# Performance work log

Hardware: AMD Instinct MI355X
Metric: run time of the kernel (lower is better)

## Reference

```python
import jax, jax.numpy as jnp
import numpy as np

NUM_CLASSES = 81
THRESHOLD = 0.5
NEGPOS_RATIO = 3
VARIANCE = (0.1, 0.2)
B, P, O = 32, 24564, 50


def point_form(pr):
    # center-form (cx,cy,w,h) -> corner-form (x1,y1,x2,y2)
    return jnp.concatenate([pr[:, :2] - pr[:, 2:] / 2, pr[:, :2] + pr[:, 2:] / 2], axis=1)


def jaccard(a, b):
    # a: [O,4] corner-form truths, b: [P,4] corner-form priors -> [O,P]
    lt = jnp.maximum(a[:, None, :2], b[None, :, :2])
    rb = jnp.minimum(a[:, None, 2:], b[None, :, 2:])
    wh = jnp.clip(rb - lt, 0.0)
    inter = wh[..., 0] * wh[..., 1]
    area_a = ((a[:, 2] - a[:, 0]) * (a[:, 3] - a[:, 1]))[:, None]
    area_b = ((b[:, 2] - b[:, 0]) * (b[:, 3] - b[:, 1]))[None, :]
    return inter / (area_a + area_b - inter)


def encode(matched, priors_cf):
    # matched: [P,4] corner-form gt; priors_cf: [P,4] center-form
    g_cxcy = ((matched[:, :2] + matched[:, 2:]) / 2 - priors_cf[:, :2]) / (VARIANCE[0] * priors_cf[:, 2:])
    g_wh = jnp.log((matched[:, 2:] - matched[:, :2]) / priors_cf[:, 2:]) / VARIANCE[1]
    return jnp.concatenate([g_cxcy, g_wh], axis=1)


def match_one(truths, labels, priors_cf, priors_pf):
    ov = jaccard(truths, priors_pf)                       # [O,P]
    best_prior_idx = jnp.argmax(ov, axis=1)               # [O] best prior per truth
    best_truth_overlap = jnp.max(ov, axis=0)              # [P]
    best_truth_idx = jnp.argmax(ov, axis=0)               # [P]
    # ensure every gt matches its best prior
    best_truth_overlap = best_truth_overlap.at[best_prior_idx].set(2.0)
    best_truth_idx = best_truth_idx.at[best_prior_idx].set(jnp.arange(truths.shape[0]))
    matches = truths[best_truth_idx]                      # [P,4]
    conf = labels[best_truth_idx] + 1                     # background = 0
    conf = jnp.where(best_truth_overlap < THRESHOLD, 0, conf)
    loc = encode(matches, priors_cf)
    return loc, conf


def setup_inputs() -> dict:
    key = jax.random.key(0)
    k1, k2, k3, k4, k5, k6, k7 = jax.random.split(key, 7)
    loc_data = jax.random.normal(k1, (B, P, 4), jnp.float32)
    conf_data = jax.random.normal(k2, (B, P, NUM_CLASSES), jnp.float32)
    cxcy = jax.random.uniform(k3, (P, 2), minval=0.05, maxval=0.95)
    wh = jax.random.uniform(k4, (P, 2), minval=0.05, maxval=0.5)
    priors = jnp.concatenate([cxcy, wh], axis=1).astype(jnp.float32)
    gc = jax.random.uniform(k5, (B, O, 2), minval=0.1, maxval=0.9)
    gwh = jax.random.uniform(k6, (B, O, 2), minval=0.05, maxval=0.4)
    boxes = jnp.clip(jnp.concatenate([gc - gwh / 2, gc + gwh / 2], axis=-1), 0.0, 1.0)
    labels = jax.random.randint(k7, (B, O), 0, NUM_CLASSES - 1).astype(jnp.float32)
    targets = jnp.concatenate([boxes, labels[..., None]], axis=-1).astype(jnp.float32)
    return {"loc_data": loc_data, "conf_data": conf_data, "priors": priors, "targets": targets}


def reference(loc_data, conf_data, priors, targets):
    truths = targets[..., :4]                              # [B,O,4]
    labels = targets[..., 4].astype(jnp.int32)             # [B,O]
    priors_pf = point_form(priors)
    loc_t, conf_t = jax.vmap(match_one, in_axes=(0, 0, None, None))(truths, labels, priors, priors_pf)
    pos = conf_t > 0                                       # [B,P]

    # localization smooth-L1 over positives (sum reduction)
    diff = loc_data - loc_t
    sl1 = jnp.where(jnp.abs(diff) < 1.0, 0.5 * diff * diff, jnp.abs(diff) - 0.5)
    loss_l = jnp.sum(sl1 * pos[..., None].astype(sl1.dtype))

    # per-anchor CE loss for hard negative mining
    lse = jax.nn.logsumexp(conf_data, axis=-1)             # [B,P]
    gathered = jnp.take_along_axis(conf_data, conf_t[..., None], axis=-1)[..., 0]
    loss_c_all = lse - gathered                            # [B,P]
    loss_c_mine = jnp.where(pos, 0.0, loss_c_all)
    loss_idx = jnp.argsort(-loss_c_mine, axis=1)
    idx_rank = jnp.argsort(loss_idx, axis=1)
    num_pos = jnp.sum(pos.astype(jnp.int32), axis=1, keepdims=True)  # [B,1]
    num_neg = jnp.minimum(NEGPOS_RATIO * num_pos, P - 1)
    neg = idx_rank < num_neg                               # [B,P]

    sel = jnp.logical_or(pos, neg)
    loss_c = jnp.sum(jnp.where(sel, loss_c_all, 0.0))

    N = jnp.sum(num_pos).astype(loss_l.dtype)
    return loss_l / N, loss_c / N
```

## Files before the change

### kernel.cpp

```cpp
#include <hip/hip_runtime.h>

#define NB 32
#define NP 24564
#define NO 50
#define NC 81
#define THR 0.5f
#define KA_CHUNK 1024
#define NCH 24

__device__ __forceinline__ float rl_f(float v, int j) {
  return __uint_as_float((unsigned)__builtin_amdgcn_readlane((int)__float_as_uint(v), j));
}
__device__ __forceinline__ float bp_f(float v, int j4) {
  return __uint_as_float((unsigned)__builtin_amdgcn_ds_bpermute(j4, (int)__float_as_uint(v)));
}


__global__ __launch_bounds__(256) void kA(
    const float* __restrict__ priors, const float* __restrict__ targets,
    unsigned long long* __restrict__ bpc,
    double* __restrict__ acc, int* __restrict__ num_pos,
    float* __restrict__ accLb, float* __restrict__ accCb,
    int* __restrict__ done) {
  __shared__ float4 s_pf[KA_CHUNK];
  __shared__ float s_t[NO * 5];
  __shared__ unsigned long long s_bp[256];
  const int b = blockIdx.y;
  const int tid = threadIdx.x;
  const int base = blockIdx.x * KA_CHUNK;

  if (blockIdx.x == 0 && b == 0) {
    if (tid < 4) acc[tid] = 0.0;
    else if (tid >= 32 && tid < 64) num_pos[tid - 32] = 0;
    else if (tid >= 64 && tid < 96) accLb[tid - 64] = 0.0f;
    else if (tid >= 96 && tid < 128) accCb[tid - 96] = 0.0f;
    else if (tid == 128) *done = 0;
  }

  for (int i = tid; i < NO * 5; i += 256) s_t[i] = targets[b * NO * 5 + i];

  #pragma unroll
  for (int k = 0; k < KA_CHUNK / 256; ++k) {
    const int p = base + k * 256 + tid;
    float4 pf;
    if (p < NP) {
      const float4 pr = ((const float4*)priors)[p];
      pf = make_float4(pr.x - pr.z * 0.5f, pr.y - pr.w * 0.5f,
                       pr.x + pr.z * 0.5f, pr.y + pr.w * 0.5f);
    } else {
      pf = make_float4(3.0f, 3.0f, 3.0f, 3.0f);
    }
    s_pf[k * 256 + tid] = pf;
  }
  __syncthreads();

  const int wv = tid >> 6;
  const int lane = tid & 63;
  unsigned long long best = 0ull;
  if (lane < NO) {
    const float tx1 = s_t[lane * 5 + 0], ty1 = s_t[lane * 5 + 1];
    const float tx2 = s_t[lane * 5 + 2], ty2 = s_t[lane * 5 + 3];
    const float area_a = (tx2 - tx1) * (ty2 - ty1);
    const int i0 = wv * 256;
    #pragma unroll 8
    for (int i = 0; i < 256; ++i) {
      const float4 q = s_pf[i0 + i];
      const float wx = fmaxf(fminf(q.z, tx2) - fmaxf(q.x, tx1), 0.0f);
      const float wy = fmaxf(fminf(q.w, ty2) - fmaxf(q.y, ty1), 0.0f);
      const float inter = wx * wy;
      const float ab = (q.z - q.x) * (q.w - q.y);
      const float iou = __fdividef(inter, area_a + ab - inter);
      const unsigned p = (unsigned)(base + i0 + i);
      const unsigned long long pk =
          (((unsigned long long)__float_as_uint(iou)) << 32) |
          (unsigned long long)(0xFFFFFFFFu - p);
      if (pk > best) best = pk;
    }
  }
  s_bp[tid] = best;
  __syncthreads();
  if (tid < NO) {
    unsigned long long m = s_bp[tid];
    unsigned long long v = s_bp[64 + tid];  if (v > m) m = v;
    v = s_bp[128 + tid];                    if (v > m) m = v;
    v = s_bp[192 + tid];                    if (v > m) m = v;
    bpc[(size_t)(b * NO + tid) * NCH + blockIdx.x] = m;
  }
}

__global__ __launch_bounds__(256) void kMS(
    const float* __restrict__ loc, const float* __restrict__ conf,
    const float* __restrict__ priors, const float* __restrict__ targets,
    const unsigned long long* __restrict__ bpc,
    float* __restrict__ mine, int* __restrict__ num_pos,
    float* __restrict__ accLb, float* __restrict__ accCb) {
  __shared__ float s_s[256];
  __shared__ int s_tpb[NO];
  __shared__ float sLw[4], sCw[4];
  __shared__ int sNw[4];
  const int tid = threadIdx.x;
  const int lane = tid & 63;
  const int b = blockIdx.y;
  const int rowbase = blockIdx.x * 256 + (tid & 192);
  const int p = rowbase + lane;
  const bool valid = (p < NP);
  const int pc = valid ? p : NP - 1;
  const size_t grow = (size_t)b * NP + pc;
  const float* tb = targets + (size_t)b * (NO * 5);

  if (tid < NO) {
    const unsigned long long* sl = bpc + (size_t)(b * NO + tid) * NCH;
    unsigned long long m = 0ull;
    #pragma unroll
    for (int c = 0; c < NCH; ++c) {
      const unsigned long long v = sl[c];
      if (v > m) m = v;
    }
    s_tpb[tid] = (int)(0xFFFFFFFFu - (unsigned)(m & 0xFFFFFFFFull));
  }

  float ttx1 = 3.f, tty1 = 3.f, ttx2 = 3.f, tty2 = 3.f, tar = 0.f, tlab = 0.f;
  if (lane < NO) {
    ttx1 = tb[lane * 5 + 0]; tty1 = tb[lane * 5 + 1];
    ttx2 = tb[lane * 5 + 2]; tty2 = tb[lane * 5 + 3];
    tlab = tb[lane * 5 + 4];
    tar = (ttx2 - ttx1) * (tty2 - tty1);
  }
  const float4 pr = ((const float4*)priors)[pc];
  const float4 ldv = ((const float4*)loc)[grow];
  const float px1 = pr.x - pr.z * 0.5f, py1 = pr.y - pr.w * 0.5f;
  const float px2 = pr.x + pr.z * 0.5f, py2 = pr.y + pr.w * 0.5f;
  const float areab = (px2 - px1) * (py2 - py1);
  __syncthreads();
  const int tpb = (lane < NO) ? s_tpb[lane] : -1;

  const int l16 = lane & 15;
  const int g4 = (lane >> 4) & 3;
  const int c0 = (4 - g4) & 3;
  const int tc = (l16 < c0) ? l16 : (c0 + 64 + (l16 - c0));
  const float* cb = conf + (size_t)b * NP * NC;

  float4 v4[8];
  float vta[8], v80[8];

  #define KMS_ROWP(ph) (cb + (size_t)((rowbase + (ph) * 4 + g4) < NP \
      ? (rowbase + (ph) * 4 + g4) : (NP - 1)) * NC)
  #define KMS_ISSUE(ph) { const float* rp_ = KMS_ROWP(ph);            \
      v4[(ph) & 7] = *(const float4*)(rp_ + c0 + 4 * l16);            \
      vta[(ph) & 7] = rp_[tc]; v80[(ph) & 7] = rp_[80]; }

  KMS_ISSUE(0) KMS_ISSUE(1) KMS_ISSUE(2)
  KMS_ISSUE(3) KMS_ISSUE(4) KMS_ISSUE(5)
  __builtin_amdgcn_sched_barrier(0);

  float bv = -1.0f;
  int bj = 0;
  #pragma unroll 2
  for (int j = 0; j < NO; ++j) {
    const float x1 = rl_f(ttx1, j), y1 = rl_f(tty1, j);
    const float x2 = rl_f(ttx2, j), y2 = rl_f(tty2, j);
    const float aa = rl_f(tar, j);
    const float wx = fmaxf(fminf(x2, px2) - fmaxf(x1, px1), 0.0f);
    const float wy = fmaxf(fminf(y2, py2) - fmaxf(y1, py1), 0.0f);
    const float inter = wx * wy;
    const float iou = __fdividef(inter, aa + areab - inter);
    if (iou > bv) { bv = iou; bj = j; }
  }

  int ovj = -1;
  unsigned long long M = __ballot((lane < NO) && ((unsigned)(tpb - rowbase) < 64u));
  while (M) {
    const int l = __ffsll((long long)M) - 1;
    M &= M - 1;
    const int r = __builtin_amdgcn_readlane(tpb, l) - rowbase;
    if (lane == r) ovj = l;
  }
  const int jm = (ovj >= 0) ? ovj : bj;
  const bool pos = valid && ((ovj >= 0) || (bv >= THR));
  const int j4 = jm << 2;
  const float lab = bp_f(tlab, j4);
  const float mx1 = bp_f(ttx1, j4), my1 = bp_f(tty1, j4);
  const float mx2 = bp_f(ttx2, j4), my2 = bp_f(tty2, j4);
  const int conft = pos ? ((int)lab + 1) : 0;

  float sl1 = 0.0f;
  if (pos) {
    const float gcx = __fdividef((mx1 + mx2) * 0.5f - pr.x, 0.1f * pr.z);
    const float gcy = __fdividef((my1 + my2) * 0.5f - pr.y, 0.1f * pr.w);
    const float gw = __logf(__fdividef(mx2 - mx1, pr.z)) * 5.0f;
    const float gh = __logf(__fdividef(my2 - my1, pr.w)) * 5.0f;
    const float d0 = ldv.x - gcx, d1 = ldv.y - gcy;
    const float d2 = ldv.z - gw, d3 = ldv.w - gh;
    #pragma unroll
    for (int q = 0; q < 4; ++q) {
      const float d = (q == 0) ? d0 : (q == 1) ? d1 : (q == 2) ? d2 : d3;
      const float a = fabsf(d);
      sl1 += (a < 1.0f) ? 0.5f * d * d : a - 0.5f;
    }
  }

  #pragma unroll
  for (int ph = 0; ph < 16; ++ph) {
    if (ph + 6 < 16) KMS_ISSUE(ph + 6)
    const float4 v = v4[ph & 7];
    float s = __expf(v.x) + __expf(v.y) + __expf(v.z) + __expf(v.w);
    s += __expf(vta[ph & 7]);
    const float e80 = __expf(v80[ph & 7]);
    s += (l16 == 0) ? e80 : 0.0f;
    s += __shfl_xor(s, 1, 64);
    s += __shfl_xor(s, 2, 64);
    s += __shfl_xor(s, 4, 64);
    s += __shfl_xor(s, 8, 64);
    if (l16 == 0) s_s[(tid & 192) + ph * 4 + g4] = s;
  }
  const float myS = s_s[tid];

  const float gval = conf[grow * NC + conft];
  const float lca = __logf(myS) - gval;

  float sumL = 0.0f, sumC = 0.0f;
  int cnt = 0;
  if (valid) {
    mine[grow] = pos ? 0.0f : fmaxf(lca, 0.0f);
    if (pos) { cnt = 1; sumC = lca; sumL = sl1; }
  }

  #pragma unroll
  for (int m = 1; m <= 32; m <<= 1) {
    sumL += __shfl_xor(sumL, m, 64);
    sumC += __shfl_xor(sumC, m, 64);
    cnt  += __shfl_xor(cnt, m, 64);
  }
  const int w = tid >> 6;
  if (lane == 0) { sLw[w] = sumL; sCw[w] = sumC; sNw[w] = cnt; }
  __syncthreads();
  if (tid == 0) {
    const float L = sLw[0] + sLw[1] + sLw[2] + sLw[3];
    const float C = sCw[0] + sCw[1] + sCw[2] + sCw[3];
    const int n = sNw[0] + sNw[1] + sNw[2] + sNw[3];
    if (L != 0.0f) atomicAdd(&accLb[b], L);
    if (C != 0.0f) atomicAdd(&accCb[b], C);
    if (n) atomicAdd(&num_pos[b], n);
  }
}

__global__ __launch_bounds__(512) void kD(
    const float* __restrict__ mine, const int* __restrict__ num_pos,
    double* __restrict__ acc, int* __restrict__ done,
    const float* __restrict__ accLb, const float* __restrict__ accCb,
    float* __restrict__ out) {
  const int b = blockIdx.x;
  const int tid = threadIdx.x;
  const uint4* vb4 = (const uint4*)(mine + (size_t)b * NP);

  unsigned vals[48];
  #pragma unroll
  for (int k = 0; k < 12; ++k) {
    const int i = tid + k * 512;
    uint4 q = make_uint4(0u, 0u, 0u, 0u);
    if (i < NP / 4) q = vb4[i];
    vals[4 * k + 0] = q.x; vals[4 * k + 1] = q.y;
    vals[4 * k + 2] = q.z; vals[4 * k + 3] = q.w;
  }

  const int K = min(3 * num_pos[b], NP - 1);

  __shared__ int s_w[2][8];
  unsigned prefix = 0u;
  int remaining = K;

  for (int bit = 30; bit >= 0; --bit) {
    const unsigned want = (prefix >> bit) | 1u;
    int cnt = 0;
    #pragma unroll
    for (int k = 0; k < 48; ++k) cnt += ((vals[k] >> bit) == want) ? 1 : 0;
    #pragma unroll
    for (int m = 32; m >= 1; m >>= 1) cnt += __shfl_xor(cnt, m, 64);
    const int buf = bit & 1;
    if ((tid & 63) == 0) s_w[buf][tid >> 6] = cnt;
    __syncthreads();
    int total = 0;
    #pragma unroll
    for (int w = 0; w < 8; ++w) total += s_w[buf][w];
    if (total >= remaining) prefix |= (1u << bit);
    else remaining -= total;
  }

  if (K > 0) {
    const float t = __uint_as_float(prefix);
    double sg = 0.0;
    int cg = 0;
    #pragma unroll
    for (int k = 0; k < 48; ++k) {
      const float f = __uint_as_float(vals[k]);
      if (f > t) { sg += (double)f; cg++; }
    }
    #pragma unroll
    for (int m = 32; m >= 1; m >>= 1) {
      sg += __shfl_xor(sg, m, 64);
      cg += __shfl_xor(cg, m, 64);
    }
    __shared__ double s_sd[8];
    __shared__ int s_sc[8];
    const int wid = tid >> 6;
    if ((tid & 63) == 0) { s_sd[wid] = sg; s_sc[wid] = cg; }
    __syncthreads();
    if (tid == 0) {
      double S = 0.0;
      int C = 0;
      for (int w = 0; w < 8; ++w) { S += s_sd[w]; C += s_sc[w]; }
      S += (double)(K - C) * (double)t;
      atomicAdd(&acc[2], S);
    }
  }

  __shared__ int s_last;
  __syncthreads();
  if (tid == 0) {
    __threadfence();
    s_last = (atomicAdd(done, 1) == NB - 1) ? 1 : 0;
  }
  __syncthreads();
  if (s_last && tid < 64) {
    int n = 0;
    float L = 0.0f, C = 0.0f;
    if (tid < NB) { n = num_pos[tid]; L = accLb[tid]; C = accCb[tid]; }
    #pragma unroll
    for (int m = 32; m >= 1; m >>= 1) {
      n += __shfl_xor(n, m, 64);
      L += __shfl_xor(L, m, 64);
      C += __shfl_xor(C, m, 64);
    }
    if (tid == 0) {
      const double S = atomicAdd(&acc[2], 0.0);
      const double Nf = (double)n;
      out[0] = (float)((double)L / Nf);
      out[1] = (float)(((double)C + S) / Nf);
    }
  }
}

extern "C" void kernel_launch(void* const* d_in, const int* in_sizes, int n_in,
                              void* d_out, int out_size, void* d_ws, size_t ws_size,
                              hipStream_t stream) {
  const float* loc     = (const float*)d_in[0];
  const float* conf    = (const float*)d_in[1];
  const float* priors  = (const float*)d_in[2];
  const float* targets = (const float*)d_in[3];
  float* out = (float*)d_out;

  char* ws = (char*)d_ws;
  double* acc   = (double*)ws;
  int* num_pos  = (int*)(ws + 32);
  float* accLb  = (float*)(ws + 160);
  float* accCb  = (float*)(ws + 288);
  int* done     = (int*)(ws + 416);
  unsigned long long* bpc = (unsigned long long*)(ws + 424);
  const size_t hdr = 424 + (size_t)NB * NO * NCH * 8;
  float* mine  = (float*)(ws + hdr);

  dim3 gA(NCH, NB);
  kA<<<gA, 256, 0, stream>>>(priors, targets, bpc,
                             acc, num_pos, accLb, accCb, done);

  dim3 gM((NP + 255) / 256, NB);
  kMS<<<gM, 256, 0, stream>>>(loc, conf, priors, targets, bpc,
                              mine, num_pos, accLb, accCb);

  kD<<<NB, 512, 0, stream>>>(mine, num_pos, acc, done, accLb, accCb, out);
}
```

Measured before the change: 142.8 us.

## Fuse hard-negative selection into match kernel via last-block-per-batch arrival counter

Removes the separate top-K selection kernel by having the last-arriving block of each batch row (tracked with a per-batch atomic arrival counter) run the radix select and final reduction inside kMS. kMS blocks grow from 256 to 512 threads to cut the number of blocks per batch to 48, and the gather of the target-class logit is hoisted earlier to overlap with the exp pass. This saves one kernel launch and lets selection for early-finishing batches overlap with other batches' matching work, at the cost of a serialized tail block per batch and larger per-block register/shared use.

```diff
diff --git a/kernel.cpp b/kernel.cpp
--- a/kernel.cpp
+++ b/kernel.cpp
@@ -21,7 +21,7 @@
     unsigned long long* __restrict__ bpc,
     double* __restrict__ acc, int* __restrict__ num_pos,
     float* __restrict__ accLb, float* __restrict__ accCb,
-    int* __restrict__ done) {
+    int* __restrict__ done, int* __restrict__ arrive) {
   __shared__ float4 s_pf[KA_CHUNK];
   __shared__ float s_t[NO * 5];
   __shared__ unsigned long long s_bp[256];
@@ -35,6 +35,7 @@
     else if (tid >= 64 && tid < 96) accLb[tid - 64] = 0.0f;
     else if (tid >= 96 && tid < 128) accCb[tid - 96] = 0.0f;
     else if (tid == 128) *done = 0;
+    else if (tid >= 160 && tid < 192) arrive[tid - 160] = 0;
   }
 
   for (int i = tid; i < NO * 5; i += 256) s_t[i] = targets[b * NO * 5 + i];
@@ -88,20 +89,27 @@
   }
 }
 
-__global__ __launch_bounds__(256) void kMS(
+__global__ __launch_bounds__(512) void kMS(
     const float* __restrict__ loc, const float* __restrict__ conf,
     const float* __restrict__ priors, const float* __restrict__ targets,
     const unsigned long long* __restrict__ bpc,
     float* __restrict__ mine, int* __restrict__ num_pos,
-    float* __restrict__ accLb, float* __restrict__ accCb) {
-  __shared__ float s_s[256];
+    float* __restrict__ accLb, float* __restrict__ accCb,
+    int* __restrict__ arrive, int* __restrict__ done,
+    double* __restrict__ acc, float* __restrict__ out) {
+  __shared__ float s_s[512];
   __shared__ int s_tpb[NO];
-  __shared__ float sLw[4], sCw[4];
-  __shared__ int sNw[4];
+  __shared__ float sLw[8], sCw[8];
+  __shared__ int sNw[8];
+  __shared__ int s_w[2][8];
+  __shared__ double s_sd[8];
+  __shared__ int s_sc[8];
+  __shared__ int s_sel, s_fin;
+
   const int tid = threadIdx.x;
   const int lane = tid & 63;
   const int b = blockIdx.y;
-  const int rowbase = blockIdx.x * 256 + (tid & 192);
+  const int rowbase = blockIdx.x * 512 + (tid & ~63);
   const int p = rowbase + lane;
   const bool valid = (p < NP);
   const int pc = valid ? p : NP - 1;
@@ -182,6 +190,8 @@
   const float mx1 = bp_f(ttx1, j4), my1 = bp_f(tty1, j4);
   const float mx2 = bp_f(ttx2, j4), my2 = bp_f(tty2, j4);
   const int conft = pos ? ((int)lab + 1) : 0;
+
+  const float gval = conf[grow * NC + conft];
 
   float sl1 = 0.0f;
   if (pos) {
@@ -211,11 +221,10 @@
     s += __shfl_xor(s, 2, 64);
     s += __shfl_xor(s, 4, 64);
     s += __shfl_xor(s, 8, 64);
-    if (l16 == 0) s_s[(tid & 192) + ph * 4 + g4] = s;
+    if (l16 == 0) s_s[(tid & ~63) + ph * 4 + g4] = s;
   }
   const float myS = s_s[tid];
 
-  const float gval = conf[grow * NC + conft];
   const float lca = __logf(myS) - gval;
 
   float sumL = 0.0f, sumC = 0.0f;
@@ -235,107 +244,100 @@
   if (lane == 0) { sLw[w] = sumL; sCw[w] = sumC; sNw[w] = cnt; }
   __syncthreads();
   if (tid == 0) {
-    const float L = sLw[0] + sLw[1] + sLw[2] + sLw[3];
-    const float C = sCw[0] + sCw[1] + sCw[2] + sCw[3];
-    const int n = sNw[0] + sNw[1] + sNw[2] + sNw[3];
+    float L = 0.0f, C = 0.0f;
+    int n = 0;
+    #pragma unroll
+    for (int q = 0; q < 8; ++q) { L += sLw[q]; C += sCw[q]; n += sNw[q]; }
     if (L != 0.0f) atomicAdd(&accLb[b], L);
     if (C != 0.0f) atomicAdd(&accCb[b], C);
     if (n) atomicAdd(&num_pos[b], n);
-  }
-}
-
-__global__ __launch_bounds__(512) void kD(
-    const float* __restrict__ mine, const int* __restrict__ num_pos,
-    double* __restrict__ acc, int* __restrict__ done,
-    const float* __restrict__ accLb, const float* __restrict__ accCb,
-    float* __restrict__ out) {
-  const int b = blockIdx.x;
-  const int tid = threadIdx.x;
-  const uint4* vb4 = (const uint4*)(mine + (size_t)b * NP);
-
-  unsigned vals[48];
-  #pragma unroll
-  for (int k = 0; k < 12; ++k) {
-    const int i = tid + k * 512;
-    uint4 q = make_uint4(0u, 0u, 0u, 0u);
-    if (i < NP / 4) q = vb4[i];
-    vals[4 * k + 0] = q.x; vals[4 * k + 1] = q.y;
-    vals[4 * k + 2] = q.z; vals[4 * k + 3] = q.w;
-  }
-
-  const int K = min(3 * num_pos[b], NP - 1);
-
-  __shared__ int s_w[2][8];
-  unsigned prefix = 0u;
-  int remaining = K;
-
-  for (int bit = 30; bit >= 0; --bit) {
-    const unsigned want = (prefix >> bit) | 1u;
-    int cnt = 0;
+    __threadfence();
+    s_sel = (atomicAdd(&arrive[b], 1) == 47) ? 1 : 0;
+  }
+  __syncthreads();
+
+  if (s_sel) {
+    __threadfence();
+    const uint4* vb4 = (const uint4*)(mine + (size_t)b * NP);
+    unsigned vals[48];
     #pragma unroll
-    for (int k = 0; k < 48; ++k) cnt += ((vals[k] >> bit) == want) ? 1 : 0;
-    #pragma unroll
-    for (int m = 32; m >= 1; m >>= 1) cnt += __shfl_xor(cnt, m, 64);
-    const int buf = bit & 1;
-    if ((tid & 63) == 0) s_w[buf][tid >> 6] = cnt;
-    __syncthreads();
-    int total = 0;
-    #pragma unroll
-    for (int w = 0; w < 8; ++w) total += s_w[buf][w];
-    if (total >= remaining) prefix |= (1u << bit);
-    else remaining -= total;
-  }
-
-  if (K > 0) {
-    const float t = __uint_as_float(prefix);
-    double sg = 0.0;
-    int cg = 0;
-    #pragma unroll
-    for (int k = 0; k < 48; ++k) {
-      const float f = __uint_as_float(vals[k]);
-      if (f > t) { sg += (double)f; cg++; }
-    }
-    #pragma unroll
-    for (int m = 32; m >= 1; m >>= 1) {
-      sg += __shfl_xor(sg, m, 64);
-      cg += __shfl_xor(cg, m, 64);
-    }
-    __shared__ double s_sd[8];
-    __shared__ int s_sc[8];
-    const int wid = tid >> 6;
-    if ((tid & 63) == 0) { s_sd[wid] = sg; s_sc[wid] = cg; }
+    for (int k = 0; k < 12; ++k) {
+      const int i = tid + k * 512;
+      uint4 q = make_uint4(0u, 0u, 0u, 0u);
+      if (i < NP / 4) q = vb4[i];
+      vals[4 * k + 0] = q.x; vals[4 * k + 1] = q.y;
+      vals[4 * k + 2] = q.z; vals[4 * k + 3] = q.w;
+    }
+    const int K = min(3 * num_pos[b], NP - 1);
+
+    unsigned prefix = 0u;
+    int remaining = K;
+    for (int bit = 30; bit >= 0; --bit) {
+      const unsigned want = (prefix >> bit) | 1u;
+      int cnt2 = 0;
+      #pragma unroll
+      for (int k = 0; k < 48; ++k) cnt2 += ((vals[k] >> bit) == want) ? 1 : 0;
+      #pragma unroll
+      for (int m = 32; m >= 1; m >>= 1) cnt2 += __shfl_xor(cnt2, m, 64);
+      const int buf = bit & 1;
+      if ((tid & 63) == 0) s_w[buf][tid >> 6] = cnt2;
+      __syncthreads();
+      int total = 0;
+      #pragma unroll
+      for (int q = 0; q < 8; ++q) total += s_w[buf][q];
+      if (total >= remaining) prefix |= (1u << bit);
+      else remaining -= total;
+    }
+
+    if (K > 0) {
+      const float t = __uint_as_float(prefix);
+      double sg = 0.0;
+      int cg = 0;
+      #pragma unroll
+      for (int k = 0; k < 48; ++k) {
+        const float f = __uint_as_float(vals[k]);
+        if (f > t) { sg += (double)f; cg++; }
+      }
+      #pragma unroll
+      for (int m = 32; m >= 1; m >>= 1) {
+        sg += __shfl_xor(sg, m, 64);
+        cg += __shfl_xor(cg, m, 64);
+      }
+      if ((tid & 63) == 0) { s_sd[tid >> 6] = sg; s_sc[tid >> 6] = cg; }
+      __syncthreads();
+      if (tid == 0) {
+        double S = 0.0;
+        int C2 = 0;
+        #pragma unroll
+        for (int q = 0; q < 8; ++q) { S += s_sd[q]; C2 += s_sc[q]; }
+        S += (double)(K - C2) * (double)t;
+        atomicAdd(&acc[2], S);
+      }
+    }
+
     __syncthreads();
     if (tid == 0) {
-      double S = 0.0;
-      int C = 0;
-      for (int w = 0; w < 8; ++w) { S += s_sd[w]; C += s_sc[w]; }
-      S += (double)(K - C) * (double)t;
-      atomicAdd(&acc[2], S);
-    }
-  }
-
-  __shared__ int s_last;
-  __syncthreads();
-  if (tid == 0) {
-    __threadfence();
-    s_last = (atomicAdd(done, 1) == NB - 1) ? 1 : 0;
-  }
-  __syncthreads();
-  if (s_last && tid < 64) {
-    int n = 0;
-    float L = 0.0f, C = 0.0f;
-    if (tid < NB) { n = num_pos[tid]; L = accLb[tid]; C = accCb[tid]; }
-    #pragma unroll
-    for (int m = 32; m >= 1; m >>= 1) {
-      n += __shfl_xor(n, m, 64);
-      L += __shfl_xor(L, m, 64);
-      C += __shfl_xor(C, m, 64);
-    }
-    if (tid == 0) {
-      const double S = atomicAdd(&acc[2], 0.0);
-      const double Nf = (double)n;
-      out[0] = (float)((double)L / Nf);
-      out[1] = (float)(((double)C + S) / Nf);
+      __threadfence();
+      s_fin = (atomicAdd(done, 1) == NB - 1) ? 1 : 0;
+    }
+    __syncthreads();
+    if (s_fin && tid < 64) {
+      __threadfence();
+      int n = 0;
+      float L = 0.0f, C = 0.0f;
+      if (tid < NB) { n = num_pos[tid]; L = accLb[tid]; C = accCb[tid]; }
+      #pragma unroll
+      for (int m = 32; m >= 1; m >>= 1) {
+        n += __shfl_xor(n, m, 64);
+        L += __shfl_xor(L, m, 64);
+        C += __shfl_xor(C, m, 64);
+      }
+      if (tid == 0) {
+        const double S = atomicAdd(&acc[2], 0.0);
+        const double Nf = (double)n;
+        out[0] = (float)((double)L / Nf);
+        out[1] = (float)(((double)C + S) / Nf);
+      }
     }
   }
 }
@@ -355,17 +357,17 @@
   float* accLb  = (float*)(ws + 160);
   float* accCb  = (float*)(ws + 288);
   int* done     = (int*)(ws + 416);
-  unsigned long long* bpc = (unsigned long long*)(ws + 424);
-  const size_t hdr = 424 + (size_t)NB * NO * NCH * 8;
+  int* arrive   = (int*)(ws + 420);
+  unsigned long long* bpc = (unsigned long long*)(ws + 552);
+  const size_t hdr = 307760;
   float* mine  = (float*)(ws + hdr);
 
   dim3 gA(NCH, NB);
   kA<<<gA, 256, 0, stream>>>(priors, targets, bpc,
-                             acc, num_pos, accLb, accCb, done);
-
-  dim3 gM((NP + 255) / 256, NB);
-  kMS<<<gM, 256, 0, stream>>>(loc, conf, priors, targets, bpc,
-                              mine, num_pos, accLb, accCb);
-
-  kD<<<NB, 512, 0, stream>>>(mine, num_pos, acc, done, accLb, accCb, out);
-}
+                             acc, num_pos, accLb, accCb, done, arrive);
+
+  dim3 gM((NP + 511) / 512, NB);
+  kMS<<<gM, 512, 0, stream>>>(loc, conf, priors, targets, bpc,
+                              mine, num_pos, accLb, accCb,
+                              arrive, done, acc, out);
+}
```

Measured after the change: 293.2 us. 105% more time.
